# Performance work log

Hardware: AMD Instinct MI355X
Metric: run time of the kernel (lower is better)

The kernel has to match this reference:

```python
import jax, jax.numpy as jnp
import numpy as np

N_NODES = 50000
N_EDGES = 800000
N_FEAT, N_HID, N_LATENT = 512, 256, 128


def spmm(rows, cols, vals, dense):
    # out[r] += vals[e] * dense[cols[e]]  -- COO SpMM via segment_sum
    gathered = dense[cols] * vals[:, None]          # [E, d]
    return jax.ops.segment_sum(gathered, rows, num_segments=N_NODES)


def setup_inputs() -> dict:
    key = jax.random.key(0)
    ks = jax.random.split(key, 8)
    x = jax.random.normal(ks[0], (N_NODES, N_FEAT), dtype=jnp.float32)
    edge_rows = jax.random.randint(ks[1], (N_EDGES,), 0, N_NODES, dtype=jnp.int32)
    edge_cols = jax.random.randint(ks[2], (N_EDGES,), 0, N_NODES, dtype=jnp.int32)
    edge_vals = jax.random.uniform(ks[3], (N_EDGES,), dtype=jnp.float32)
    # Glorot-style init like the torch GraphConvolution
    W1 = jax.random.normal(ks[4], (N_FEAT, N_HID), dtype=jnp.float32) / np.sqrt(N_FEAT)
    b1 = jnp.zeros((N_HID,), dtype=jnp.float32)
    W2 = jax.random.normal(ks[5], (N_HID, N_LATENT), dtype=jnp.float32) / np.sqrt(N_HID)
    b2 = jnp.zeros((N_LATENT,), dtype=jnp.float32)
    return {"x": x, "edge_rows": edge_rows, "edge_cols": edge_cols,
            "edge_vals": edge_vals, "W1": W1, "b1": b1, "W2": W2, "b2": b2}


def reference(x, edge_rows, edge_cols, edge_vals, W1, b1, W2, b2):
    # layer 1: relu(adj @ (x @ W1) + b1)
    h = spmm(edge_rows, edge_cols, edge_vals, x @ W1) + b1
    h = jax.nn.relu(h)
    # layer 2: relu(adj @ (h @ W2) + b2)
    z = spmm(edge_rows, edge_cols, edge_vals, h @ W2) + b2
    return jax.nn.relu(z)
```

## Files before the change

### kernel.cpp

```cpp
#include <hip/hip_runtime.h>
#include <hip/hip_bf16.h>


typedef __attribute__((ext_vector_type(8))) short bf16x8;
typedef __attribute__((ext_vector_type(4))) float f32x4;

#define NN 50000
#define NE 800000
#define NF 512
#define NH 256
#define NL 128
#define NB ((NN + 255) / 256)

static __device__ __forceinline__ unsigned short f2bf(float f) {
  union { float f; unsigned int u; } v; v.f = f;
  unsigned int r = v.u + 0x7fffu + ((v.u >> 16) & 1u);
  return (unsigned short)(r >> 16);
}
static __device__ __forceinline__ float bf2f(unsigned short u) {
  union { unsigned int u; float f; } v; v.u = (unsigned int)u << 16;
  return v.f;
}

static __device__ __forceinline__ unsigned int pkbf(float lo, float hi) {
  unsigned int r;
  asm("v_cvt_pk_bf16_f32 %0, %1, %2" : "=v"(r) : "v"(lo), "v"(hi));
  return r;
}
static __device__ __forceinline__ uint4 pk8(float4 a, float4 b) {
  uint4 o;
  o.x = pkbf(a.x, a.y); o.y = pkbf(a.z, a.w);
  o.z = pkbf(b.x, b.y); o.w = pkbf(b.z, b.w);
  return o;
}

static __device__ __forceinline__ void gll16(const void* g, void* l) {
  __builtin_amdgcn_global_load_lds(
      (const __attribute__((address_space(1))) void*)g,
      (__attribute__((address_space(3))) void*)l, 16, 0, 0);
}

extern "C" __global__ void k_hist(const int* __restrict__ rows, int* __restrict__ counts, int n) {
  int i = blockIdx.x * 256 + threadIdx.x;
  if (i < n) atomicAdd(&counts[rows[i]], 1);
}

extern "C" __global__ __launch_bounds__(256) void k_blocksum(
    const int* __restrict__ counts, int* __restrict__ bsum, int n) {
  __shared__ int s[256];
  int t = threadIdx.x;
  int i = blockIdx.x * 256 + t;
  s[t] = (i < n) ? counts[i] : 0;
  __syncthreads();
  for (int off = 128; off > 0; off >>= 1) {
    if (t < off) s[t] += s[t + off];
    __syncthreads();
  }
  if (t == 0) bsum[blockIdx.x] = s[0];
}

extern "C" __global__ __launch_bounds__(256) void k_scansums(
    const int* __restrict__ bsum, int* __restrict__ bpre, int* __restrict__ rp, int nb, int n) {
  __shared__ int s[256];
  int t = threadIdx.x;
  int v = (t < nb) ? bsum[t] : 0;
  s[t] = v;
  __syncthreads();
  for (int off = 1; off < 256; off <<= 1) {
    int u = (t >= off) ? s[t - off] : 0;
    __syncthreads();
    s[t] += u;
    __syncthreads();
  }
  if (t < nb) bpre[t] = s[t] - v;
  if (t == 255) rp[n] = s[255];
}

extern "C" __global__ __launch_bounds__(256) void k_scanfin(
    const int* __restrict__ counts, const int* __restrict__ bpre,
    int* __restrict__ rp, int* __restrict__ cur, int n) {
  __shared__ int s[256];
  int t = threadIdx.x;
  int i = blockIdx.x * 256 + t;
  int c = (i < n) ? counts[i] : 0;
  s[t] = c;
  __syncthreads();
  for (int off = 1; off < 256; off <<= 1) {
    int u = (t >= off) ? s[t - off] : 0;
    __syncthreads();
    s[t] += u;
    __syncthreads();
  }
  if (i < n) {
    int e = bpre[blockIdx.x] + s[t] - c;
    rp[i] = e;
    cur[i] = e;
  }
}

extern "C" __global__ void k_scatter(const int* __restrict__ rows, const int* __restrict__ cols,
    const float* __restrict__ vals, int* __restrict__ cur, int2* __restrict__ ep, int n) {
  int i = blockIdx.x * 256 + threadIdx.x;
  if (i < n) {
    int p = atomicAdd(&cur[rows[i]], 1);
    int2 e; e.x = cols[i]; e.y = __float_as_int(vals[i]);
    ep[p] = e;
  }
}

extern "C" __global__ void k_transcast(const float* __restrict__ w, unsigned short* __restrict__ wt,
                                       int K, int N) {
  int k = blockIdx.x; int n = threadIdx.x;
  wt[(size_t)n * K + k] = f2bf(w[(size_t)k * N + n]);
}

extern "C" __global__ __launch_bounds__(256, 2) void k_gemm1(
    const float* __restrict__ A, const unsigned short* __restrict__ BT,
    unsigned short* __restrict__ C) {
  __shared__ __align__(16) unsigned short sB[64 * 512];
  int tid = threadIdx.x;
  int lane = tid & 63, wid = tid >> 6;
  int l15 = lane & 15, lq = lane >> 4;
  int bm = blockIdx.x * 64, bn = blockIdx.y * 64;

#pragma unroll
  for (int j = 0; j < 16; ++j) {
    int u = tid + 256 * j;
    int row = u >> 6, cu = u & 63;
    int g = cu ^ (row & 7);
    gll16(BT + (size_t)(bn + row) * NF + g * 8, &sB[u * 8]);
  }

  int arow = bm + wid * 16 + l15; if (arow >= NN) arow = NN - 1;
  const float* ap = A + (size_t)arow * NF + lq * 8;

  float4 apf[4][2];
#pragma unroll
  for (int p = 0; p < 4; ++p) {
    apf[p][0] = *(const float4*)(ap + p * 32);
    apf[p][1] = *(const float4*)(ap + p * 32 + 4);
  }

  __syncthreads();

  f32x4 acc[4];
#pragma unroll
  for (int i = 0; i < 4; ++i) acc[i] = (f32x4){0.f, 0.f, 0.f, 0.f};

#pragma unroll
  for (int p = 0; p < 16; ++p) {
    bf16x8 bfr[4];
#pragma unroll
    for (int nt = 0; nt < 4; ++nt) {
      int c = nt * 16 + l15;
      int u = (p * 4 + lq) ^ (c & 7);
      bfr[nt] = *(const bf16x8*)(&sB[c * 512 + u * 8]);
    }
    union { uint4 u; bf16x8 v; } cv;
    cv.u = pk8(apf[p & 3][0], apf[p & 3][1]);
    bf16x8 af = cv.v;
    if (p < 12) {
      apf[p & 3][0] = *(const float4*)(ap + (p + 4) * 32);
      apf[p & 3][1] = *(const float4*)(ap + (p + 4) * 32 + 4);
    }
#pragma unroll
    for (int nt = 0; nt < 4; ++nt)
      acc[nt] = __builtin_amdgcn_mfma_f32_16x16x32_bf16(af, bfr[nt], acc[nt], 0, 0, 0);
  }

#pragma unroll
  for (int nt = 0; nt < 4; ++nt) {
#pragma unroll
    for (int r = 0; r < 4; ++r) {
      int gr = bm + wid * 16 + lq * 4 + r;
      if (gr < NN) {
        int gc = bn + nt * 16 + l15;
        C[(size_t)gr * NH + gc] = f2bf(acc[nt][r]);
      }
    }
  }
}

extern "C" __global__ __launch_bounds__(256, 2) void k_gemm2(
    const unsigned short* __restrict__ Ah, const unsigned short* __restrict__ BT,
    unsigned short* __restrict__ C) {
  __shared__ __align__(16) unsigned short sB[128 * 256];
  int tid = threadIdx.x;
  int lane = tid & 63, wid = tid >> 6;
  int l15 = lane & 15, lq = lane >> 4;
  int bm = blockIdx.x * 64;

#pragma unroll
  for (int j = 0; j < 16; ++j) {
    int u = tid + 256 * j;
    int row = u >> 5, cu = u & 31;
    int g = cu ^ (row & 7);
    gll16(BT + (size_t)row * NH + g * 8, &sB[u * 8]);
  }

  int arow = bm + wid * 16 + l15; if (arow >= NN) arow = NN - 1;
  const unsigned short* ap = Ah + (size_t)arow * NH + lq * 8;

  bf16x8 apf[4];
#pragma unroll
  for (int p = 0; p < 4; ++p) apf[p] = *(const bf16x8*)(ap + p * 32);

  __syncthreads();

  f32x4 acc[8];
#pragma unroll
  for (int i = 0; i < 8; ++i) acc[i] = (f32x4){0.f, 0.f, 0.f, 0.f};

#pragma unroll
  for (int p = 0; p < 8; ++p) {
    bf16x8 bfr[8];
#pragma unroll
    for (int nt = 0; nt < 8; ++nt) {
      int c = nt * 16 + l15;
      int u = (p * 4 + lq) ^ (c & 7);
      bfr[nt] = *(const bf16x8*)(&sB[c * 256 + u * 8]);
    }
    bf16x8 af = apf[p & 3];
    if (p < 4) apf[p & 3] = *(const bf16x8*)(ap + (p + 4) * 32);
#pragma unroll
    for (int nt = 0; nt < 8; ++nt)
      acc[nt] = __builtin_amdgcn_mfma_f32_16x16x32_bf16(af, bfr[nt], acc[nt], 0, 0, 0);
  }

#pragma unroll
  for (int nt = 0; nt < 8; ++nt) {
#pragma unroll
    for (int r = 0; r < 4; ++r) {
      int gr = bm + wid * 16 + lq * 4 + r;
      if (gr < NN) {
        int gc = nt * 16 + l15;
        C[(size_t)gr * NL + gc] = f2bf(acc[nt][r]);
      }
    }
  }
}

extern "C" __global__ __launch_bounds__(256) void k_spmm256(
    const int* __restrict__ rp, const int2* __restrict__ ep,
    const unsigned short* __restrict__ src, const float* __restrict__ bias,
    ushort4* __restrict__ out) {
  int row = blockIdx.x * 4 + (threadIdx.x >> 6);
  int lane = threadIdx.x & 63;
  if (row >= NN) return;
  int e0 = __builtin_amdgcn_readfirstlane(rp[row]);
  int e1 = __builtin_amdgcn_readfirstlane(rp[row + 1]);
  const ushort4* srcv = (const ushort4*)src;
  float4 acc = {0.f, 0.f, 0.f, 0.f};
  int e = e0;
  for (; e + 8 <= e1; e += 8) {
    int2 p[8]; ushort4 g[8];
#pragma unroll
    for (int j = 0; j < 8; ++j) p[j] = ep[e + j];
#pragma unroll
    for (int j = 0; j < 8; ++j) g[j] = srcv[(size_t)p[j].x * (NH / 4) + lane];
#pragma unroll
    for (int j = 0; j < 8; ++j) {
      float v = __int_as_float(p[j].y);
      acc.x = fmaf(v, bf2f(g[j].x), acc.x); acc.y = fmaf(v, bf2f(g[j].y), acc.y);
      acc.z = fmaf(v, bf2f(g[j].z), acc.z); acc.w = fmaf(v, bf2f(g[j].w), acc.w);
    }
  }
  for (; e + 4 <= e1; e += 4) {
    int2 p[4]; ushort4 g[4];
#pragma unroll
    for (int j = 0; j < 4; ++j) p[j] = ep[e + j];
#pragma unroll
    for (int j = 0; j < 4; ++j) g[j] = srcv[(size_t)p[j].x * (NH / 4) + lane];
#pragma unroll
    for (int j = 0; j < 4; ++j) {
      float v = __int_as_float(p[j].y);
      acc.x = fmaf(v, bf2f(g[j].x), acc.x); acc.y = fmaf(v, bf2f(g[j].y), acc.y);
      acc.z = fmaf(v, bf2f(g[j].z), acc.z); acc.w = fmaf(v, bf2f(g[j].w), acc.w);
    }
  }
  for (; e < e1; ++e) {
    int2 p = ep[e];
    float v = __int_as_float(p.y);
    ushort4 g = srcv[(size_t)p.x * (NH / 4) + lane];
    acc.x = fmaf(v, bf2f(g.x), acc.x); acc.y = fmaf(v, bf2f(g.y), acc.y);
    acc.z = fmaf(v, bf2f(g.z), acc.z); acc.w = fmaf(v, bf2f(g.w), acc.w);
  }
  float4 b = ((const float4*)bias)[lane];
  ushort4 o;
  o.x = f2bf(fmaxf(acc.x + b.x, 0.f));
  o.y = f2bf(fmaxf(acc.y + b.y, 0.f));
  o.z = f2bf(fmaxf(acc.z + b.z, 0.f));
  o.w = f2bf(fmaxf(acc.w + b.w, 0.f));
  out[(size_t)row * (NH / 4) + lane] = o;
}

extern "C" __global__ __launch_bounds__(256) void k_spmm128(
    const int* __restrict__ rp, const int2* __restrict__ ep,
    const unsigned short* __restrict__ src, const float* __restrict__ bias,
    float2* __restrict__ out) {
  int row = blockIdx.x * 4 + (threadIdx.x >> 6);
  int lane = threadIdx.x & 63;
  if (row >= NN) return;
  int e0 = __builtin_amdgcn_readfirstlane(rp[row]);
  int e1 = __builtin_amdgcn_readfirstlane(rp[row + 1]);
  const ushort2* srcv = (const ushort2*)src;
  float2 acc = {0.f, 0.f};
  int e = e0;
  for (; e + 8 <= e1; e += 8) {
    int2 p[8]; ushort2 g[8];
#pragma unroll
    for (int j = 0; j < 8; ++j) p[j] = ep[e + j];
#pragma unroll
    for (int j = 0; j < 8; ++j) g[j] = srcv[(size_t)p[j].x * (NL / 2) + lane];
#pragma unroll
    for (int j = 0; j < 8; ++j) {
      float v = __int_as_float(p[j].y);
      acc.x = fmaf(v, bf2f(g[j].x), acc.x); acc.y = fmaf(v, bf2f(g[j].y), acc.y);
    }
  }
  for (; e + 4 <= e1; e += 4) {
    int2 p[4]; ushort2 g[4];
#pragma unroll
    for (int j = 0; j < 4; ++j) p[j] = ep[e + j];
#pragma unroll
    for (int j = 0; j < 4; ++j) g[j] = srcv[(size_t)p[j].x * (NL / 2) + lane];
#pragma unroll
    for (int j = 0; j < 4; ++j) {
      float v = __int_as_float(p[j].y);
      acc.x = fmaf(v, bf2f(g[j].x), acc.x); acc.y = fmaf(v, bf2f(g[j].y), acc.y);
    }
  }
  for (; e < e1; ++e) {
    int2 p = ep[e];
    float v = __int_as_float(p.y);
    ushort2 g = srcv[(size_t)p.x * (NL / 2) + lane];
    acc.x = fmaf(v, bf2f(g.x), acc.x); acc.y = fmaf(v, bf2f(g.y), acc.y);
  }
  float2 b = ((const float2*)bias)[lane];
  float2 o;
  o.x = fmaxf(acc.x + b.x, 0.f);
  o.y = fmaxf(acc.y + b.y, 0.f);
  out[(size_t)row * (NL / 2) + lane] = o;
}

extern "C" void kernel_launch(void* const* d_in, const int* in_sizes, int n_in,
                              void* d_out, int out_size, void* d_ws, size_t ws_size,
                              hipStream_t stream) {
  const float* x   = (const float*)d_in[0];
  const int* erow  = (const int*)d_in[1];
  const int* ecol  = (const int*)d_in[2];
  const float* ev  = (const float*)d_in[3];
  const float* W1  = (const float*)d_in[4];
  const float* b1  = (const float*)d_in[5];
  const float* W2  = (const float*)d_in[6];
  const float* b2  = (const float*)d_in[7];

  char* ws = (char*)d_ws;
  unsigned short* xwb = (unsigned short*)(ws + 0);
  unsigned short* hbf = (unsigned short*)(ws + 25600000);
  unsigned short* hwb = (unsigned short*)(ws + 51200000);
  unsigned short* w1t = (unsigned short*)(ws + 64000000);
  unsigned short* w2t = (unsigned short*)(ws + 64262144);
  int* rp    = (int*)(ws + 64327680);
  int* cur   = (int*)(ws + 64528384);
  int* cnt   = (int*)(ws + 64729088);
  int* bsum  = (int*)(ws + 64929792);
  int* bpre  = (int*)(ws + 64930816);
  int2* ep   = (int2*)(ws + 64931840);

  hipMemsetAsync(cnt, 0, NN * sizeof(int), stream);
  k_hist<<<NE / 256, 256, 0, stream>>>(erow, cnt, NE);
  k_blocksum<<<NB, 256, 0, stream>>>(cnt, bsum, NN);
  k_scansums<<<1, 256, 0, stream>>>(bsum, bpre, rp, NB, NN);
  k_scanfin<<<NB, 256, 0, stream>>>(cnt, bpre, rp, cur, NN);
  k_scatter<<<NE / 256, 256, 0, stream>>>(erow, ecol, ev, cur, ep, NE);

  k_transcast<<<NF, NH, 0, stream>>>(W1, w1t, NF, NH);
  k_gemm1<<<dim3((NN + 63) / 64, 4), 256, 0, stream>>>(x, w1t, xwb);
  k_spmm256<<<NN / 4, 256, 0, stream>>>(rp, ep, xwb, b1, (ushort4*)hbf);

  k_transcast<<<NH, NL, 0, stream>>>(W2, w2t, NH, NL);
  k_gemm2<<<(NN + 63) / 64, 256, 0, stream>>>(hbf, w2t, hwb);
  k_spmm128<<<NN / 4, 256, 0, stream>>>(rp, ep, hwb, b2, (float2*)d_out);
}
```

Measured before the change: 415.5 us.

## Compute full N=256 per gemm1 block with double-buffered B tiles in LDS

The first GEMM previously launched 4 column blocks per row tile, so each block reread and reconverted the same fp32 rows of x. Now each block covers all 256 output columns. It converts its A fragment to bf16 once and keeps it in registers, then streams 32-column slices of W1ᵀ through two LDS buffers with async loads overlapping the MFMAs. This cuts global reads of x by four, at the cost of many more accumulator and A registers, which may lower occupancy, and more barriers.

```diff
diff --git a/kernel.cpp b/kernel.cpp
--- a/kernel.cpp
+++ b/kernel.cpp
@@ -117,65 +117,89 @@
 extern "C" __global__ __launch_bounds__(256, 2) void k_gemm1(
     const float* __restrict__ A, const unsigned short* __restrict__ BT,
     unsigned short* __restrict__ C) {
-  __shared__ __align__(16) unsigned short sB[64 * 512];
+  __shared__ __align__(16) unsigned short sB[2][32 * 512];
   int tid = threadIdx.x;
   int lane = tid & 63, wid = tid >> 6;
   int l15 = lane & 15, lq = lane >> 4;
-  int bm = blockIdx.x * 64, bn = blockIdx.y * 64;
-
-#pragma unroll
-  for (int j = 0; j < 16; ++j) {
-    int u = tid + 256 * j;
-    int row = u >> 6, cu = u & 63;
-    int g = cu ^ (row & 7);
-    gll16(BT + (size_t)(bn + row) * NF + g * 8, &sB[u * 8]);
-  }
+  int bm = blockIdx.x * 64;
+
+  auto issueB = [&](int q, int b) {
+#pragma unroll
+    for (int j = 0; j < 8; ++j) {
+      int u = tid + 256 * j;
+      int c = u >> 6, cu = u & 63;
+      int g = cu ^ (c & 7);
+      gll16(BT + (size_t)(q * 32 + c) * NF + g * 8, &sB[b][u * 8]);
+    }
+  };
 
   int arow = bm + wid * 16 + l15; if (arow >= NN) arow = NN - 1;
   const float* ap = A + (size_t)arow * NF + lq * 8;
 
+  issueB(0, 0);
   float4 apf[4][2];
 #pragma unroll
   for (int p = 0; p < 4; ++p) {
     apf[p][0] = *(const float4*)(ap + p * 32);
     apf[p][1] = *(const float4*)(ap + p * 32 + 4);
   }
-
-  __syncthreads();
-
-  f32x4 acc[4];
-#pragma unroll
-  for (int i = 0; i < 4; ++i) acc[i] = (f32x4){0.f, 0.f, 0.f, 0.f};
+  __syncthreads();
+  issueB(1, 1);
+
+  bf16x8 abf[16];
+  f32x4 acc[16];
+#pragma unroll
+  for (int i = 0; i < 16; ++i) acc[i] = (f32x4){0.f, 0.f, 0.f, 0.f};
 
 #pragma unroll
   for (int p = 0; p < 16; ++p) {
-    bf16x8 bfr[4];
-#pragma unroll
-    for (int nt = 0; nt < 4; ++nt) {
+    bf16x8 bfr[2];
+#pragma unroll
+    for (int nt = 0; nt < 2; ++nt) {
       int c = nt * 16 + l15;
       int u = (p * 4 + lq) ^ (c & 7);
-      bfr[nt] = *(const bf16x8*)(&sB[c * 512 + u * 8]);
+      bfr[nt] = *(const bf16x8*)(&sB[0][c * 512 + u * 8]);
     }
     union { uint4 u; bf16x8 v; } cv;
     cv.u = pk8(apf[p & 3][0], apf[p & 3][1]);
-    bf16x8 af = cv.v;
+    abf[p] = cv.v;
     if (p < 12) {
       apf[p & 3][0] = *(const float4*)(ap + (p + 4) * 32);
       apf[p & 3][1] = *(const float4*)(ap + (p + 4) * 32 + 4);
     }
 #pragma unroll
-    for (int nt = 0; nt < 4; ++nt)
-      acc[nt] = __builtin_amdgcn_mfma_f32_16x16x32_bf16(af, bfr[nt], acc[nt], 0, 0, 0);
-  }
-
-#pragma unroll
-  for (int nt = 0; nt < 4; ++nt) {
+    for (int nt = 0; nt < 2; ++nt)
+      acc[nt] = __builtin_amdgcn_mfma_f32_16x16x32_bf16(abf[p], bfr[nt], acc[nt], 0, 0, 0);
+  }
+  __syncthreads();
+
+#pragma unroll
+  for (int q = 1; q < 8; ++q) {
+    if (q < 7) issueB(q + 1, (q + 1) & 1);
+#pragma unroll
+    for (int p = 0; p < 16; ++p) {
+      bf16x8 bfr[2];
+#pragma unroll
+      for (int nt = 0; nt < 2; ++nt) {
+        int c = nt * 16 + l15;
+        int u = (p * 4 + lq) ^ (c & 7);
+        bfr[nt] = *(const bf16x8*)(&sB[q & 1][c * 512 + u * 8]);
+      }
+#pragma unroll
+      for (int nt = 0; nt < 2; ++nt)
+        acc[q * 2 + nt] = __builtin_amdgcn_mfma_f32_16x16x32_bf16(abf[p], bfr[nt], acc[q * 2 + nt], 0, 0, 0);
+    }
+    if (q < 7) __syncthreads();
+  }
+
+#pragma unroll
+  for (int t = 0; t < 16; ++t) {
 #pragma unroll
     for (int r = 0; r < 4; ++r) {
       int gr = bm + wid * 16 + lq * 4 + r;
       if (gr < NN) {
-        int gc = bn + nt * 16 + l15;
-        C[(size_t)gr * NH + gc] = f2bf(acc[nt][r]);
+        int gc = t * 16 + l15;
+        C[(size_t)gr * NH + gc] = f2bf(acc[t][r]);
       }
     }
   }
@@ -376,7 +400,7 @@
   k_scatter<<<NE / 256, 256, 0, stream>>>(erow, ecol, ev, cur, ep, NE);
 
   k_transcast<<<NF, NH, 0, stream>>>(W1, w1t, NF, NH);
-  k_gemm1<<<dim3((NN + 63) / 64, 4), 256, 0, stream>>>(x, w1t, xwb);
+  k_gemm1<<<(NN + 63) / 64, 256, 0, stream>>>(x, w1t, xwb);
   k_spmm256<<<NN / 4, 256, 0, stream>>>(rp, ep, xwb, b1, (ushort4*)hbf);
 
   k_transcast<<<NH, NL, 0, stream>>>(W2, w2t, NH, NL);
```

Result: faster. 382.2 us (-8.0%).
